# Optimization experiments

Hardware: AMD Instinct MI355X
Metric: run time of the kernel (lower is better)

The kernel has to match this reference:

```python
import jax, jax.numpy as jnp
import numpy as np

EPS = 1e-12  # matches tf l2_normalize epsilon behavior closely enough for testing

def setup_inputs() -> dict:
    key = jax.random.key(0)
    k1, k2 = jax.random.split(key)
    B, M, D = 512, 65536, 512
    context = jax.random.normal(k1, (B, D), dtype=jnp.float32)
    memory = jax.random.normal(k2, (M, D), dtype=jnp.float32)
    return {"context": context, "memory": memory}

def reference(context, memory):
    # tf.keras.losses.cosine_similarity returns NEGATIVE cosine similarity:
    # sim[b,m] = -sum(l2norm(context[b]) * l2norm(memory[m]))
    ctx_n = context / jnp.sqrt(jnp.maximum(jnp.sum(context * context, axis=-1, keepdims=True), EPS))
    mem_n = memory / jnp.sqrt(jnp.maximum(jnp.sum(memory * memory, axis=-1, keepdims=True), EPS))
    sim = -jnp.einsum('bd,md->bm', ctx_n, mem_n)  # [B, M]
    best = jnp.argmin(sim, axis=-1)               # [B], = argmax cosine
    # recall: gather then expand_dims(axis=0) -> [1, B, D]
    return memory[best][None, :, :]
```

## Files before the change

### kernel.cpp

```cpp
#include <hip/hip_runtime.h>
#include <hip/hip_bf16.h>
#include <stdint.h>

#define D_DIM 512
#define B_CTX 512
#define M_MEM 65536
#define BM 128
#define BB 128
#define BBW 256
#define BK 32
#define GBK 32
#define NIT (D_DIM / GBK)
#define LDSPAD 40
#define DELTA_COS 2.5e-3f
#define LISTCAP 2048
#define CVT_MEM_BLOCKS (M_MEM / 32)
#define CVT_BLOCKS (CVT_MEM_BLOCKS + B_CTX / 32)

typedef __attribute__((ext_vector_type(8))) short short8;
typedef __attribute__((ext_vector_type(4))) float floatx4;

__device__ __forceinline__ uint32_t f32_order(float s) {
    uint32_t u = __float_as_uint(s);
    return (u & 0x80000000u) ? ~u : (u | 0x80000000u);
}
__device__ __forceinline__ float f32_unorder(uint32_t v) {
    uint32_t u = (v & 0x80000000u) ? (v & 0x7FFFFFFFu) : ~v;
    return __uint_as_float(u);
}
__device__ __forceinline__ uint32_t pack_bf16_rtn(float a, float b) {
    uint32_t ua = __float_as_uint(a) + 0x8000u;
    uint32_t ub = __float_as_uint(b) + 0x8000u;
    return (ua >> 16) | (ub & 0xFFFF0000u);
}

typedef const __attribute__((address_space(1))) void gv_t;
typedef __attribute__((address_space(3))) void lv_t;
__device__ __forceinline__ void gload_lds16(const uint16_t* g, uint16_t* l) {
    __builtin_amdgcn_global_load_lds((gv_t*)g, (lv_t*)l, 16, 0, 0);
}

__device__ __forceinline__ bool probe_isbf(const void* memv, int* s_bf, int t) {
    if (t == 0) *s_bf = 0;
    __syncthreads();
    if (t < 64) {
        int s = 0;
        #pragma unroll
        for (int i = 0; i < 8; ++i) {
            uint32_t u = ((const uint32_t*)memv)[t * 8 + i];
            uint32_t e = (u >> 7) & 0xFFu;
            s += (e >= 96u && e <= 144u) ? 1 : 0;
        }
        atomicAdd(s_bf, s);
    }
    __syncthreads();
    return (*s_bf > 256);
}

__global__ void detect_init(const uint32_t* __restrict__ mem_raw,
                            uint32_t* __restrict__ flag) {
    __shared__ int cnt;
    if (threadIdx.x == 0) cnt = 0;
    __syncthreads();
    int s = 0;
    #pragma unroll
    for (int i = 0; i < 8; ++i) {
        uint32_t u = mem_raw[threadIdx.x * 8 + i];
        uint32_t e = (u >> 7) & 0xFFu;
        s += (e >= 96u && e <= 144u) ? 1 : 0;
    }
    atomicAdd(&cnt, s);
    __syncthreads();
    if (threadIdx.x == 0) *flag = (cnt > 256) ? 1u : 0u;
}

__global__ __launch_bounds__(256) void convert_scale(const void* __restrict__ ctxv,
                                                     const void* __restrict__ memv,
                                                     uint16_t* __restrict__ mem_s,
                                                     uint16_t* __restrict__ ctx_b) {
    __shared__ int s_bf;
    const int t = threadIdx.x;
    const bool isbf = probe_isbf(memv, &s_bf, t);
    const int lane = t & 63;
    const int w = t >> 6;
    if (blockIdx.x < CVT_MEM_BLOCKS) {
        const int r0 = (blockIdx.x * 4 + w) * 8;
        float x[8][8];
        if (isbf) {
            #pragma unroll
            for (int i = 0; i < 8; ++i) {
                uint4 v = *((const uint4*)((const uint16_t*)memv + (size_t)(r0 + i) * D_DIM) + lane);
                uint32_t ww[4] = {v.x, v.y, v.z, v.w};
                #pragma unroll
                for (int j = 0; j < 4; ++j) {
                    x[i][2 * j]     = __uint_as_float(ww[j] << 16);
                    x[i][2 * j + 1] = __uint_as_float(ww[j] & 0xFFFF0000u);
                }
            }
        } else {
            #pragma unroll
            for (int i = 0; i < 8; ++i) {
                const float4* p = (const float4*)((const float*)memv + (size_t)(r0 + i) * D_DIM) + lane * 2;
                float4 a = p[0], bq = p[1];
                x[i][0] = a.x; x[i][1] = a.y; x[i][2] = a.z; x[i][3] = a.w;
                x[i][4] = bq.x; x[i][5] = bq.y; x[i][6] = bq.z; x[i][7] = bq.w;
            }
        }
        float nsq[8];
        #pragma unroll
        for (int i = 0; i < 8; ++i) {
            float s = 0.f;
            #pragma unroll
            for (int j = 0; j < 8; ++j) s = fmaf(x[i][j], x[i][j], s);
            nsq[i] = s;
        }
        #pragma unroll
        for (int o = 32; o; o >>= 1)
            #pragma unroll
            for (int i = 0; i < 8; ++i)
                nsq[i] += __shfl_xor(nsq[i], o, 64);
        #pragma unroll
        for (int i = 0; i < 8; ++i) {
            const float invn = rsqrtf(fmaxf(nsq[i], 1e-12f));
            uint4 ov;
            ov.x = pack_bf16_rtn(x[i][0] * invn, x[i][1] * invn);
            ov.y = pack_bf16_rtn(x[i][2] * invn, x[i][3] * invn);
            ov.z = pack_bf16_rtn(x[i][4] * invn, x[i][5] * invn);
            ov.w = pack_bf16_rtn(x[i][6] * invn, x[i][7] * invn);
            *((uint4*)(mem_s + (size_t)(r0 + i) * D_DIM) + lane) = ov;
        }
    } else {
        const int r0 = ((blockIdx.x - CVT_MEM_BLOCKS) * 4 + w) * 8;
        #pragma unroll
        for (int i = 0; i < 8; ++i) {
            uint4 ov;
            if (isbf) {
                ov = *((const uint4*)((const uint16_t*)ctxv + (size_t)(r0 + i) * D_DIM) + lane);
            } else {
                const float4* p = (const float4*)((const float*)ctxv + (size_t)(r0 + i) * D_DIM) + lane * 2;
                float4 a = p[0], bq = p[1];
                ov.x = pack_bf16_rtn(a.x, a.y);
                ov.y = pack_bf16_rtn(a.z, a.w);
                ov.z = pack_bf16_rtn(bq.x, bq.y);
                ov.w = pack_bf16_rtn(bq.z, bq.w);
            }
            *((uint4*)(ctx_b + (size_t)(r0 + i) * D_DIM) + lane) = ov;
        }
    }
}

#define STAGE3(buf, kofs)                                                          \
    do {                                                                           \
        gload_lds16(ga  + (kofs), &at[buf][0][0] + (size_t)((w << 6)) * 8);        \
        gload_lds16(gb0 + (kofs), &bt[buf][0][0] + (size_t)((w << 6)) * 8);        \
        gload_lds16(gb1 + (kofs), &bt[buf][0][0] + (size_t)(512 + (w << 6)) * 8);  \
    } while (0)

__global__ __launch_bounds__(512, 4) void score_mfma(const uint16_t* __restrict__ A,
                                                     const uint16_t* __restrict__ Bc,
                                                     uint32_t* __restrict__ tmax,
                                                     int coarse) {
    __shared__ __align__(16) uint16_t at[3][BM][GBK];
    __shared__ __align__(16) uint16_t bt[3][BBW][GBK];
    __shared__ uint32_t s_gbest[8][BBW];

    const int h  = blockIdx.y * gridDim.x + blockIdx.x;
    const int v  = (h & 7) * 128 + (h >> 3);
    const int bxp = v & 1;
    const int byp = v >> 1;

    const int t    = threadIdx.x;
    const int b0   = bxp * BBW;
    const int m0   = byp * BM;
    const int lane = t & 63;
    const int w    = t >> 6;
    const int wm   = w >> 2;
    const int wb   = w & 3;
    const int quad = lane >> 4;
    const int l15  = lane & 15;
    const int scol_sw = (((t & 3) ^ ((t >> 3) & 3)) << 3);
    const int rc = ((quad ^ ((l15 >> 1) & 3)) << 3);

    const uint16_t* ga  = A  + (size_t)(m0 + (t >> 2)) * D_DIM + scol_sw;
    const uint16_t* gb0 = Bc + (size_t)(b0 + (t >> 2)) * D_DIM + scol_sw;
    const uint16_t* gb1 = gb0 + (size_t)128 * D_DIM;

    floatx4 acc[4][4];
    #pragma unroll
    for (int i = 0; i < 4; ++i)
        #pragma unroll
        for (int j = 0; j < 4; ++j)
            acc[i][j] = (floatx4){0.f, 0.f, 0.f, 0.f};

    STAGE3(0, 0);

    #pragma unroll
    for (int it = 0; it < NIT; ++it) {
        const int cur = it % 3;
        if (it < NIT - 1) STAGE3((it + 1) % 3, (it + 1) * GBK);
        if (it < NIT - 1) asm volatile("s_waitcnt vmcnt(3)" ::: "memory");
        else              asm volatile("s_waitcnt vmcnt(0)" ::: "memory");
        __builtin_amdgcn_sched_barrier(0);
        __builtin_amdgcn_s_barrier();
        __builtin_amdgcn_sched_barrier(0);

        short8 af[4], bg[4];
        #pragma unroll
        for (int i = 0; i < 4; ++i)
            af[i] = *(const short8*)&at[cur][wm * 64 + i * 16 + l15][rc];
        #pragma unroll
        for (int j = 0; j < 4; ++j)
            bg[j] = *(const short8*)&bt[cur][wb * 64 + j * 16 + l15][rc];
        __builtin_amdgcn_s_setprio(1);
        #pragma unroll
        for (int i = 0; i < 4; ++i)
            #pragma unroll
            for (int j = 0; j < 4; ++j)
                acc[i][j] = __builtin_amdgcn_mfma_f32_16x16x32_bf16(af[i], bg[j], acc[i][j], 0, 0, 0);
        __builtin_amdgcn_s_setprio(0);
    }

    #pragma unroll
    for (int i = 0; i < 4; ++i)
        #pragma unroll
        for (int j = 0; j < 4; ++j) {
            uint32_t k = 0;
            #pragma unroll
            for (int r = 0; r < 4; ++r) {
                uint32_t kk = f32_order(acc[i][j][r]);
                k = kk > k ? kk : k;
            }
            uint32_t o1 = __shfl_xor(k, 16, 64); k = o1 > k ? o1 : k;
            uint32_t o2 = __shfl_xor(k, 32, 64); k = o2 > k ? o2 : k;
            if (quad == 0) s_gbest[wm * 4 + i][wb * 64 + j * 16 + l15] = k;
        }
    __syncthreads();

    if (!coarse) {
        const int G0 = byp * 8;
        for (int e = t; e < 8 * BBW; e += 512) {
            const int col = e >> 3, g = e & 7;
            tmax[(size_t)(b0 + col) * 4096 + G0 + g] = s_gbest[g][col];
        }
    } else {
        if (t < BBW) {
            uint32_t k = s_gbest[0][t];
            #pragma unroll
            for (int g = 1; g < 8; ++g) k = s_gbest[g][t] > k ? s_gbest[g][t] : k;
            tmax[(size_t)(b0 + t) * 512 + byp] = k;
        }
    }
}

__global__ __launch_bounds__(256) void score_phase1(const void* __restrict__ ctxv,
                                                    const void* __restrict__ memv,
                                                    const uint32_t* __restrict__ flag,
                                                    uint32_t* __restrict__ tmax,
                                                    int coarse) {
    __shared__ __align__(16) uint16_t at[BM][LDSPAD];
    __shared__ __align__(16) uint16_t bt[BB][LDSPAD];
    __shared__ float s_nsq[BM];
    __shared__ uint32_t s_gbest[8][BB];

    const int t    = threadIdx.x;
    const int b0   = blockIdx.x * BB;
    const int m0   = blockIdx.y * BM;
    const int lane = t & 63;
    const int w    = t >> 6;
    const int wm   = w >> 1;
    const int wb   = w & 1;
    const int quad = lane >> 4;
    const int l15  = lane & 15;
    const int srow = t >> 2;
    const int scol = (t & 3) * 8;

    floatx4 acc[4][4];
    #pragma unroll
    for (int i = 0; i < 4; ++i)
        #pragma unroll
        for (int j = 0; j < 4; ++j)
            acc[i][j] = (floatx4){0.f, 0.f, 0.f, 0.f};

    float nsq0 = 0.f, nsq1 = 0.f;
    const bool isbf = (*flag != 0u);

    for (int k0 = 0; k0 < D_DIM; k0 += BK) {
        __syncthreads();
        if (isbf) {
            const uint16_t* mp = (const uint16_t*)memv;
            const uint16_t* cp = (const uint16_t*)ctxv;
            uint4 va0 = *(const uint4*)(mp + (size_t)(m0 + srow) * D_DIM + k0 + scol);
            uint4 va1 = *(const uint4*)(mp + (size_t)(m0 + srow + 64) * D_DIM + k0 + scol);
            uint4 vb0 = *(const uint4*)(cp + (size_t)(b0 + srow) * D_DIM + k0 + scol);
            uint4 vb1 = *(const uint4*)(cp + (size_t)(b0 + srow + 64) * D_DIM + k0 + scol);
            *(uint4*)&at[srow][scol] = va0;
            *(uint4*)&at[srow + 64][scol] = va1;
            *(uint4*)&bt[srow][scol] = vb0;
            *(uint4*)&bt[srow + 64][scol] = vb1;
            uint32_t wa0[4] = {va0.x, va0.y, va0.z, va0.w};
            uint32_t wa1[4] = {va1.x, va1.y, va1.z, va1.w};
            #pragma unroll
            for (int i = 0; i < 4; ++i) {
                float a = __uint_as_float(wa0[i] << 16);
                float b = __uint_as_float(wa0[i] & 0xFFFF0000u);
                nsq0 = fmaf(a, a, nsq0); nsq0 = fmaf(b, b, nsq0);
                float c = __uint_as_float(wa1[i] << 16);
                float d = __uint_as_float(wa1[i] & 0xFFFF0000u);
                nsq1 = fmaf(c, c, nsq1); nsq1 = fmaf(d, d, nsq1);
            }
        } else {
            const float* mp = (const float*)memv;
            const float* cp = (const float*)ctxv;
            const float4* pa0 = (const float4*)(mp + (size_t)(m0 + srow) * D_DIM + k0 + scol);
            const float4* pa1 = (const float4*)(mp + (size_t)(m0 + srow + 64) * D_DIM + k0 + scol);
            const float4* pb0 = (const float4*)(cp + (size_t)(b0 + srow) * D_DIM + k0 + scol);
            const float4* pb1 = (const float4*)(cp + (size_t)(b0 + srow + 64) * D_DIM + k0 + scol);
            float4 a0 = pa0[0], a1 = pa0[1], a2 = pa1[0], a3 = pa1[1];
            float4 c0 = pb0[0], c1 = pb0[1], c2 = pb1[0], c3 = pb1[1];
            uint4 va0 = {pack_bf16_rtn(a0.x, a0.y), pack_bf16_rtn(a0.z, a0.w),
                         pack_bf16_rtn(a1.x, a1.y), pack_bf16_rtn(a1.z, a1.w)};
            uint4 va1 = {pack_bf16_rtn(a2.x, a2.y), pack_bf16_rtn(a2.z, a2.w),
                         pack_bf16_rtn(a3.x, a3.y), pack_bf16_rtn(a3.z, a3.w)};
            uint4 vb0 = {pack_bf16_rtn(c0.x, c0.y), pack_bf16_rtn(c0.z, c0.w),
                         pack_bf16_rtn(c1.x, c1.y), pack_bf16_rtn(c1.z, c1.w)};
            uint4 vb1 = {pack_bf16_rtn(c2.x, c2.y), pack_bf16_rtn(c2.z, c2.w),
                         pack_bf16_rtn(c3.x, c3.y), pack_bf16_rtn(c3.z, c3.w)};
            *(uint4*)&at[srow][scol] = va0;
            *(uint4*)&at[srow + 64][scol] = va1;
            *(uint4*)&bt[srow][scol] = vb0;
            *(uint4*)&bt[srow + 64][scol] = vb1;
            nsq0 = fmaf(a0.x, a0.x, nsq0); nsq0 = fmaf(a0.y, a0.y, nsq0);
            nsq0 = fmaf(a0.z, a0.z, nsq0); nsq0 = fmaf(a0.w, a0.w, nsq0);
            nsq0 = fmaf(a1.x, a1.x, nsq0); nsq0 = fmaf(a1.y, a1.y, nsq0);
            nsq0 = fmaf(a1.z, a1.z, nsq0); nsq0 = fmaf(a1.w, a1.w, nsq0);
            nsq1 = fmaf(a2.x, a2.x, nsq1); nsq1 = fmaf(a2.y, a2.y, nsq1);
            nsq1 = fmaf(a2.z, a2.z, nsq1); nsq1 = fmaf(a2.w, a2.w, nsq1);
            nsq1 = fmaf(a3.x, a3.x, nsq1); nsq1 = fmaf(a3.y, a3.y, nsq1);
            nsq1 = fmaf(a3.z, a3.z, nsq1); nsq1 = fmaf(a3.w, a3.w, nsq1);
        }
        __syncthreads();

        short8 af[4], bg[4];
        #pragma unroll
        for (int i = 0; i < 4; ++i)
            af[i] = *(const short8*)&at[wm * 64 + i * 16 + l15][quad * 8];
        #pragma unroll
        for (int j = 0; j < 4; ++j)
            bg[j] = *(const short8*)&bt[wb * 64 + j * 16 + l15][quad * 8];

        #pragma unroll
        for (int i = 0; i < 4; ++i)
            #pragma unroll
            for (int j = 0; j < 4; ++j)
                acc[i][j] = __builtin_amdgcn_mfma_f32_16x16x32_bf16(af[i], bg[j], acc[i][j], 0, 0, 0);
    }

    nsq0 += __shfl_xor(nsq0, 1, 64); nsq0 += __shfl_xor(nsq0, 2, 64);
    nsq1 += __shfl_xor(nsq1, 1, 64); nsq1 += __shfl_xor(nsq1, 2, 64);
    __syncthreads();
    if ((t & 3) == 0) { s_nsq[srow] = nsq0; s_nsq[srow + 64] = nsq1; }
    __syncthreads();

    float invn[4][4];
    #pragma unroll
    for (int i = 0; i < 4; ++i)
        #pragma unroll
        for (int r = 0; r < 4; ++r)
            invn[i][r] = rsqrtf(fmaxf(s_nsq[wm * 64 + i * 16 + quad * 4 + r], 1e-12f));

    #pragma unroll
    for (int i = 0; i < 4; ++i)
        #pragma unroll
        for (int j = 0; j < 4; ++j) {
            uint32_t k = 0;
            #pragma unroll
            for (int r = 0; r < 4; ++r) {
                uint32_t kk = f32_order(acc[i][j][r] * invn[i][r]);
                k = kk > k ? kk : k;
            }
            uint32_t o1 = __shfl_xor(k, 16, 64); k = o1 > k ? o1 : k;
            uint32_t o2 = __shfl_xor(k, 32, 64); k = o2 > k ? o2 : k;
            if (quad == 0) s_gbest[wm * 4 + i][wb * 64 + j * 16 + l15] = k;
        }
    __syncthreads();

    if (!coarse) {
        const int G0 = blockIdx.y * 8;
        for (int e = t; e < 8 * BB; e += 256) {
            const int col = e >> 3, g = e & 7;
            tmax[(size_t)(b0 + col) * 4096 + G0 + g] = s_gbest[g][col];
        }
    } else {
        if (t < BB) {
            uint32_t k = s_gbest[0][t];
            #pragma unroll
            for (int g = 1; g < 8; ++g) k = s_gbest[g][t] > k ? s_gbest[g][t] : k;
            tmax[(size_t)(b0 + t) * 512 + blockIdx.y] = k;
        }
    }
}

__global__ __launch_bounds__(256) void phase2(const void* __restrict__ ctxv,
                                              const void* __restrict__ memv,
                                              const uint32_t* __restrict__ tmax,
                                              void* __restrict__ outv,
                                              int ngrp, int gshift) {
    __shared__ float s_ctx[D_DIM];
    __shared__ int s_list[LISTCAP];
    __shared__ int s_cnt;
    __shared__ int s_bf;
    __shared__ uint32_t s_red[4];
    __shared__ float s_cn[4];
    __shared__ double s_d[4], s_n[4];
    __shared__ int s_m[4];
    __shared__ int s_bestm;

    const int b = blockIdx.x;
    const int t = threadIdx.x;
    const int lane = t & 63;
    const int w = t >> 6;
    const int gmask = (1 << gshift) - 1;

    if (t == 0) s_cnt = 0;
    const bool isbf = probe_isbf(memv, &s_bf, t);

    if (isbf) {
        if (t < 64) {
            uint4 v = *((const uint4*)((const uint16_t*)ctxv + (size_t)b * D_DIM) + t);
            uint32_t ww[4] = {v.x, v.y, v.z, v.w};
            #pragma unroll
            for (int i = 0; i < 4; ++i) {
                s_ctx[t * 8 + 2 * i]     = __uint_as_float(ww[i] << 16);
                s_ctx[t * 8 + 2 * i + 1] = __uint_as_float(ww[i] & 0xFFFF0000u);
            }
        }
    } else {
        if (t < 128)
            ((float4*)s_ctx)[t] = ((const float4*)((const float*)ctxv + (size_t)b * D_DIM))[t];
    }
    __syncthreads();

    float cs = s_ctx[t] * s_ctx[t] + s_ctx[t + 256] * s_ctx[t + 256];
    #pragma unroll
    for (int o = 32; o; o >>= 1) cs += __shfl_xor(cs, o, 64);
    if (lane == 0) s_cn[w] = cs;

    const uint32_t* tk = tmax + (size_t)b * ngrp;
    uint32_t kv[16];
    uint32_t km = 0;
    const bool fine = (ngrp == 4096);
    if (fine) {
        #pragma unroll
        for (int i = 0; i < 16; ++i) kv[i] = tk[t + (i << 8)];
        #pragma unroll
        for (int i = 0; i < 16; ++i) km = kv[i] > km ? kv[i] : km;
    } else {
        #pragma unroll
        for (int i = 0; i < 2; ++i) kv[i] = tk[t + (i << 8)];
        km = kv[0] > kv[1] ? kv[0] : kv[1];
    }
    #pragma unroll
    for (int o = 32; o; o >>= 1) { uint32_t ot = __shfl_xor(km, o, 64); km = ot > km ? ot : km; }
    if (lane == 0) s_red[w] = km;
    __syncthreads();
    uint32_t kbest = s_red[0];
    #pragma unroll
    for (int i = 1; i < 4; ++i) kbest = s_red[i] > kbest ? s_red[i] : kbest;
    const float cnorm = sqrtf(s_cn[0] + s_cn[1] + s_cn[2] + s_cn[3]);
    const uint32_t keyT = f32_order(f32_unorder(kbest) - DELTA_COS * cnorm);

    if (fine) {
        #pragma unroll
        for (int i = 0; i < 16; ++i)
            if (kv[i] >= keyT) {
                int idx = atomicAdd(&s_cnt, 1);
                if (idx < LISTCAP) s_list[idx] = t + (i << 8);
            }
    } else {
        #pragma unroll
        for (int i = 0; i < 2; ++i)
            if (kv[i] >= keyT) {
                int idx = atomicAdd(&s_cnt, 1);
                if (idx < LISTCAP) s_list[idx] = t + (i << 8);
            }
    }
    __syncthreads();
    int cnt = s_cnt; if (cnt > LISTCAP) cnt = LISTCAP;
    const int total = cnt << gshift;

    double bd = -1.0e300, bn = 1.0;
    double bp = bd * 1.0e300;
    int bm = 0x7FFFFFFF;
    const float* cb = s_ctx + lane * 8;

    for (int base = w * 2; base < total; base += 8) {
        const bool has1 = (base + 1 < total);
        const int ia = base, ib = has1 ? base + 1 : base;
        const int ma = (s_list[ia >> gshift] << gshift) + (ia & gmask);
        const int mb = (s_list[ib >> gshift] << gshift) + (ib & gmask);
        double d0 = 0.0, n0 = 0.0, d1 = 0.0, n1 = 0.0;
        if (isbf) {
            uint4 va = *((const uint4*)((const uint16_t*)memv + (size_t)ma * D_DIM) + lane);
            uint4 vb = *((const uint4*)((const uint16_t*)memv + (size_t)mb * D_DIM) + lane);
            uint32_t wa[4] = {va.x, va.y, va.z, va.w};
            uint32_t wbv[4] = {vb.x, vb.y, vb.z, vb.w};
            #pragma unroll
            for (int i = 0; i < 4; ++i) {
                float a0 = __uint_as_float(wa[i] << 16);
                float a1 = __uint_as_float(wa[i] & 0xFFFF0000u);
                d0 += (double)a0 * (double)cb[2 * i];
                d0 += (double)a1 * (double)cb[2 * i + 1];
                n0 += (double)a0 * (double)a0 + (double)a1 * (double)a1;
                float b0v = __uint_as_float(wbv[i] << 16);
                float b1v = __uint_as_float(wbv[i] & 0xFFFF0000u);
                d1 += (double)b0v * (double)cb[2 * i];
                d1 += (double)b1v * (double)cb[2 * i + 1];
                n1 += (double)b0v * (double)b0v + (double)b1v * (double)b1v;
            }
        } else {
            const float4* pa = (const float4*)((const float*)memv + (size_t)ma * D_DIM) + lane * 2;
            const float4* pb = (const float4*)((const float*)memv + (size_t)mb * D_DIM) + lane * 2;
            float4 a0 = pa[0], a1 = pa[1], b0v = pb[0], b1v = pb[1];
            float xa[8] = {a0.x, a0.y, a0.z, a0.w, a1.x, a1.y, a1.z, a1.w};
            float xb[8] = {b0v.x, b0v.y, b0v.z, b0v.w, b1v.x, b1v.y, b1v.z, b1v.w};
            #pragma unroll
            for (int i = 0; i < 8; ++i) {
                d0 += (double)xa[i] * (double)cb[i];
                n0 += (double)xa[i] * (double)xa[i];
                d1 += (double)xb[i] * (double)cb[i];
                n1 += (double)xb[i] * (double)xb[i];
            }
        }
        #pragma unroll
        for (int o = 32; o; o >>= 1) {
            d0 += __shfl_xor(d0, o, 64);
            n0 += __shfl_xor(n0, o, 64);
            d1 += __shfl_xor(d1, o, 64);
            n1 += __shfl_xor(n1, o, 64);
        }
        double p0 = d0 * fabs(d0);
        double lhs = p0 * bn, rhs = bp * n0;
        if (lhs > rhs || (lhs == rhs && ma < bm)) { bd = d0; bn = n0; bp = p0; bm = ma; }
        if (has1) {
            double p1 = d1 * fabs(d1);
            double lhs1 = p1 * bn, rhs1 = bp * n1;
            if (lhs1 > rhs1 || (lhs1 == rhs1 && mb < bm)) { bd = d1; bn = n1; bp = p1; bm = mb; }
        }
    }
    if (lane == 0) { s_d[w] = bd; s_n[w] = bn; s_m[w] = bm; }
    __syncthreads();
    if (t == 0) {
        double cd = s_d[0], cn2 = s_n[0], cp = cd * fabs(cd);
        int cm = s_m[0];
        #pragma unroll
        for (int i = 1; i < 4; ++i) {
            double pd = s_d[i], pn = s_n[i], pp = pd * fabs(pd);
            double lhs = pp * cn2, rhs = cp * pn;
            if (lhs > rhs || (lhs == rhs && s_m[i] < cm)) { cd = pd; cn2 = pn; cp = pp; cm = s_m[i]; }
        }
        s_bestm = cm;
    }
    __syncthreads();
    const int mbest = s_bestm;
    if (isbf) {
        if (t < 64)
            ((uint4*)((uint16_t*)outv + (size_t)b * D_DIM))[t] =
                ((const uint4*)((const uint16_t*)memv + (size_t)mbest * D_DIM))[t];
    } else {
        if (t < 128)
            ((float4*)((float*)outv + (size_t)b * D_DIM))[t] =
                ((const float4*)((const float*)memv + (size_t)mbest * D_DIM))[t];
    }
}

extern "C" void kernel_launch(void* const* d_in, const int* in_sizes, int n_in,
                              void* d_out, int out_size, void* d_ws, size_t ws_size,
                              hipStream_t stream) {
    const void* ctx = d_in[0];
    const void* mem = d_in[1];
    if (in_sizes[0] > in_sizes[1]) { ctx = d_in[1]; mem = d_in[0]; }

    const size_t fineBytes   = (size_t)B_CTX * 4096 * 4;
    const size_t coarseBytes = (size_t)B_CTX * 512 * 4;
    const size_t ctxBytes    = (size_t)B_CTX * D_DIM * 2;
    const size_t memBytes    = (size_t)M_MEM * D_DIM * 2;
    const size_t fastBytes   = fineBytes + 256 + ctxBytes + memBytes;

    if (ws_size >= fastBytes) {
        uint32_t* tmax  = (uint32_t*)d_ws;
        uint16_t* ctx_b = (uint16_t*)((char*)d_ws + fineBytes + 256);
        uint16_t* mem_s = (uint16_t*)((char*)d_ws + fineBytes + 256 + ctxBytes);
        dim3 grid(B_CTX / BBW, M_MEM / BM);
        convert_scale<<<CVT_BLOCKS, 256, 0, stream>>>(ctx, mem, mem_s, ctx_b);
        score_mfma<<<grid, 512, 0, stream>>>(mem_s, ctx_b, tmax, 0);
        phase2<<<B_CTX, 256, 0, stream>>>(ctx, mem, tmax, d_out, 4096, 4);
    } else if (ws_size >= fineBytes + 256) {
        uint32_t* tmax = (uint32_t*)d_ws;
        uint32_t* flag = (uint32_t*)((char*)d_ws + fineBytes);
        dim3 grid(B_CTX / BB, M_MEM / BM);
        detect_init<<<1, 64, 0, stream>>>((const uint32_t*)mem, flag);
        score_phase1<<<grid, 256, 0, stream>>>(ctx, mem, flag, tmax, 0);
        phase2<<<B_CTX, 256, 0, stream>>>(ctx, mem, tmax, d_out, 4096, 4);
    } else {
        uint32_t* tmax = (uint32_t*)d_ws;
        uint32_t* flag = (uint32_t*)((char*)d_ws + coarseBytes);
        dim3 grid(B_CTX / BB, M_MEM / BM);
        detect_init<<<1, 64, 0, stream>>>((const uint32_t*)mem, flag);
        score_phase1<<<grid, 256, 0, stream>>>(ctx, mem, flag, tmax, 1);
        phase2<<<B_CTX, 256, 0, stream>>>(ctx, mem, tmax, d_out, 512, 7);
    }
}
```

Measured before the change: 263.5 us.

## Fuse memory normalization and bf16 conversion into the MFMA scoring kernel

Removes the separate pass that normalized the memory rows and wrote a bf16 copy to workspace. The scoring kernel now reads raw memory (fp32 or bf16), converts each tile to bf16 in registers and stores it to LDS, and accumulates the squared row norms along the way. It then scales the accumulated dot products by the inverse norm before the max reduction. This drops the 64MB intermediate write and read-back, but the raw memory is now read once per context-column block. The kernel also replaces the triple-buffered async LDS pipeline with a double buffer synchronised every iteration.

```diff
diff --git a/kernel.cpp b/kernel.cpp
--- a/kernel.cpp
+++ b/kernel.cpp
@@ -14,8 +14,6 @@
 #define LDSPAD 40
 #define DELTA_COS 2.5e-3f
 #define LISTCAP 2048
-#define CVT_MEM_BLOCKS (M_MEM / 32)
-#define CVT_BLOCKS (CVT_MEM_BLOCKS + B_CTX / 32)
 
 typedef __attribute__((ext_vector_type(8))) short short8;
 typedef __attribute__((ext_vector_type(4))) float floatx4;
@@ -74,117 +72,70 @@
     if (threadIdx.x == 0) *flag = (cnt > 256) ? 1u : 0u;
 }
 
-__global__ __launch_bounds__(256) void convert_scale(const void* __restrict__ ctxv,
-                                                     const void* __restrict__ memv,
-                                                     uint16_t* __restrict__ mem_s,
-                                                     uint16_t* __restrict__ ctx_b) {
+__global__ __launch_bounds__(256) void convert_ctx(const void* __restrict__ ctxv,
+                                                   const void* __restrict__ memv,
+                                                   uint16_t* __restrict__ ctx_b) {
     __shared__ int s_bf;
     const int t = threadIdx.x;
     const bool isbf = probe_isbf(memv, &s_bf, t);
     const int lane = t & 63;
     const int w = t >> 6;
-    if (blockIdx.x < CVT_MEM_BLOCKS) {
-        const int r0 = (blockIdx.x * 4 + w) * 8;
-        float x[8][8];
+    const int r0 = (blockIdx.x * 4 + w) * 8;
+    #pragma unroll
+    for (int i = 0; i < 8; ++i) {
+        uint4 ov;
         if (isbf) {
-            #pragma unroll
-            for (int i = 0; i < 8; ++i) {
-                uint4 v = *((const uint4*)((const uint16_t*)memv + (size_t)(r0 + i) * D_DIM) + lane);
-                uint32_t ww[4] = {v.x, v.y, v.z, v.w};
-                #pragma unroll
-                for (int j = 0; j < 4; ++j) {
-                    x[i][2 * j]     = __uint_as_float(ww[j] << 16);
-                    x[i][2 * j + 1] = __uint_as_float(ww[j] & 0xFFFF0000u);
-                }
-            }
+            ov = *((const uint4*)((const uint16_t*)ctxv + (size_t)(r0 + i) * D_DIM) + lane);
         } else {
-            #pragma unroll
-            for (int i = 0; i < 8; ++i) {
-                const float4* p = (const float4*)((const float*)memv + (size_t)(r0 + i) * D_DIM) + lane * 2;
-                float4 a = p[0], bq = p[1];
-                x[i][0] = a.x; x[i][1] = a.y; x[i][2] = a.z; x[i][3] = a.w;
-                x[i][4] = bq.x; x[i][5] = bq.y; x[i][6] = bq.z; x[i][7] = bq.w;
-            }
-        }
-        float nsq[8];
-        #pragma unroll
-        for (int i = 0; i < 8; ++i) {
-            float s = 0.f;
-            #pragma unroll
-            for (int j = 0; j < 8; ++j) s = fmaf(x[i][j], x[i][j], s);
-            nsq[i] = s;
-        }
-        #pragma unroll
-        for (int o = 32; o; o >>= 1)
-            #pragma unroll
-            for (int i = 0; i < 8; ++i)
-                nsq[i] += __shfl_xor(nsq[i], o, 64);
-        #pragma unroll
-        for (int i = 0; i < 8; ++i) {
-            const float invn = rsqrtf(fmaxf(nsq[i], 1e-12f));
-            uint4 ov;
-            ov.x = pack_bf16_rtn(x[i][0] * invn, x[i][1] * invn);
-            ov.y = pack_bf16_rtn(x[i][2] * invn, x[i][3] * invn);
-            ov.z = pack_bf16_rtn(x[i][4] * invn, x[i][5] * invn);
-            ov.w = pack_bf16_rtn(x[i][6] * invn, x[i][7] * invn);
-            *((uint4*)(mem_s + (size_t)(r0 + i) * D_DIM) + lane) = ov;
-        }
-    } else {
-        const int r0 = ((blockIdx.x - CVT_MEM_BLOCKS) * 4 + w) * 8;
-        #pragma unroll
-        for (int i = 0; i < 8; ++i) {
-            uint4 ov;
-            if (isbf) {
-                ov = *((const uint4*)((const uint16_t*)ctxv + (size_t)(r0 + i) * D_DIM) + lane);
-            } else {
-                const float4* p = (const float4*)((const float*)ctxv + (size_t)(r0 + i) * D_DIM) + lane * 2;
-                float4 a = p[0], bq = p[1];
-                ov.x = pack_bf16_rtn(a.x, a.y);
-                ov.y = pack_bf16_rtn(a.z, a.w);
-                ov.z = pack_bf16_rtn(bq.x, bq.y);
-                ov.w = pack_bf16_rtn(bq.z, bq.w);
-            }
-            *((uint4*)(ctx_b + (size_t)(r0 + i) * D_DIM) + lane) = ov;
-        }
-    }
-}
-
-#define STAGE3(buf, kofs)                                                          \
-    do {                                                                           \
-        gload_lds16(ga  + (kofs), &at[buf][0][0] + (size_t)((w << 6)) * 8);        \
-        gload_lds16(gb0 + (kofs), &bt[buf][0][0] + (size_t)((w << 6)) * 8);        \
-        gload_lds16(gb1 + (kofs), &bt[buf][0][0] + (size_t)(512 + (w << 6)) * 8);  \
-    } while (0)
-
-__global__ __launch_bounds__(512, 4) void score_mfma(const uint16_t* __restrict__ A,
-                                                     const uint16_t* __restrict__ Bc,
-                                                     uint32_t* __restrict__ tmax,
-                                                     int coarse) {
-    __shared__ __align__(16) uint16_t at[3][BM][GBK];
-    __shared__ __align__(16) uint16_t bt[3][BBW][GBK];
+            const float4* p = (const float4*)((const float*)ctxv + (size_t)(r0 + i) * D_DIM) + lane * 2;
+            float4 a = p[0], bq = p[1];
+            ov.x = pack_bf16_rtn(a.x, a.y);
+            ov.y = pack_bf16_rtn(a.z, a.w);
+            ov.z = pack_bf16_rtn(bq.x, bq.y);
+            ov.w = pack_bf16_rtn(bq.z, bq.w);
+        }
+        *((uint4*)(ctx_b + (size_t)(r0 + i) * D_DIM) + lane) = ov;
+    }
+}
+
+__global__ __launch_bounds__(512, 4) void score_fused(const void* __restrict__ memv,
+                                                      const uint16_t* __restrict__ Bc,
+                                                      uint32_t* __restrict__ tmax,
+                                                      int coarse) {
+    __shared__ __align__(16) uint16_t at[2][BM][GBK];
+    __shared__ __align__(16) uint16_t bt[2][BBW][GBK];
     __shared__ uint32_t s_gbest[8][BBW];
+    __shared__ float s_nsq[BM];
+    __shared__ int s_bf;
+
+    const int t = threadIdx.x;
+    const bool isbf = probe_isbf(memv, &s_bf, t);
 
     const int h  = blockIdx.y * gridDim.x + blockIdx.x;
     const int v  = (h & 7) * 128 + (h >> 3);
     const int bxp = v & 1;
     const int byp = v >> 1;
-
-    const int t    = threadIdx.x;
-    const int b0   = bxp * BBW;
-    const int m0   = byp * BM;
+    const int b0  = bxp * BBW;
+    const int m0  = byp * BM;
     const int lane = t & 63;
     const int w    = t >> 6;
     const int wm   = w >> 2;
     const int wb   = w & 3;
     const int quad = lane >> 4;
     const int l15  = lane & 15;
+
+    const int arow = t >> 2;
+    const int achk = t & 3;
+    const int aswz = achk ^ ((arow >> 1) & 3);
     const int scol_sw = (((t & 3) ^ ((t >> 3) & 3)) << 3);
     const int rc = ((quad ^ ((l15 >> 1) & 3)) << 3);
 
-    const uint16_t* ga  = A  + (size_t)(m0 + (t >> 2)) * D_DIM + scol_sw;
     const uint16_t* gb0 = Bc + (size_t)(b0 + (t >> 2)) * D_DIM + scol_sw;
     const uint16_t* gb1 = gb0 + (size_t)128 * D_DIM;
-
+    const float*    gaf = (const float*)memv + (size_t)(m0 + arow) * D_DIM + achk * 8;
+    const uint16_t* gab = (const uint16_t*)memv + (size_t)(m0 + arow) * D_DIM + achk * 8;
+
+    float nsq = 0.f;
     floatx4 acc[4][4];
     #pragma unroll
     for (int i = 0; i < 4; ++i)
@@ -192,18 +143,38 @@
         for (int j = 0; j < 4; ++j)
             acc[i][j] = (floatx4){0.f, 0.f, 0.f, 0.f};
 
-    STAGE3(0, 0);
+    {
+        gload_lds16(gb0, &bt[0][0][0] + (size_t)(w << 6) * 8);
+        gload_lds16(gb1, &bt[0][0][0] + (size_t)(512 + (w << 6)) * 8);
+        uint4 av;
+        float xs[8];
+        if (isbf) {
+            av = *(const uint4*)gab;
+            uint32_t ww[4] = {av.x, av.y, av.z, av.w};
+            #pragma unroll
+            for (int j = 0; j < 4; ++j) {
+                xs[2 * j]     = __uint_as_float(ww[j] << 16);
+                xs[2 * j + 1] = __uint_as_float(ww[j] & 0xFFFF0000u);
+            }
+        } else {
+            float4 fa = *(const float4*)gaf;
+            float4 fb = *(const float4*)(gaf + 4);
+            xs[0] = fa.x; xs[1] = fa.y; xs[2] = fa.z; xs[3] = fa.w;
+            xs[4] = fb.x; xs[5] = fb.y; xs[6] = fb.z; xs[7] = fb.w;
+            av.x = pack_bf16_rtn(xs[0], xs[1]);
+            av.y = pack_bf16_rtn(xs[2], xs[3]);
+            av.z = pack_bf16_rtn(xs[4], xs[5]);
+            av.w = pack_bf16_rtn(xs[6], xs[7]);
+        }
+        #pragma unroll
+        for (int j = 0; j < 8; ++j) nsq = fmaf(xs[j], xs[j], nsq);
+        *(uint4*)&at[0][arow][aswz * 8] = av;
+        __syncthreads();
+    }
 
     #pragma unroll
     for (int it = 0; it < NIT; ++it) {
-        const int cur = it % 3;
-        if (it < NIT - 1) STAGE3((it + 1) % 3, (it + 1) * GBK);
-        if (it < NIT - 1) asm volatile("s_waitcnt vmcnt(3)" ::: "memory");
-        else              asm volatile("s_waitcnt vmcnt(0)" ::: "memory");
-        __builtin_amdgcn_sched_barrier(0);
-        __builtin_amdgcn_s_barrier();
-        __builtin_amdgcn_sched_barrier(0);
-
+        const int cur = it & 1;
         short8 af[4], bg[4];
         #pragma unroll
         for (int i = 0; i < 4; ++i)
@@ -211,6 +182,23 @@
         #pragma unroll
         for (int j = 0; j < 4; ++j)
             bg[j] = *(const short8*)&bt[cur][wb * 64 + j * 16 + l15][rc];
+
+        uint4 av;
+        float xs[8];
+        if (it < NIT - 1) {
+            const int ko = (it + 1) * GBK;
+            gload_lds16(gb0 + ko, &bt[cur ^ 1][0][0] + (size_t)(w << 6) * 8);
+            gload_lds16(gb1 + ko, &bt[cur ^ 1][0][0] + (size_t)(512 + (w << 6)) * 8);
+            if (isbf) {
+                av = *(const uint4*)(gab + ko);
+            } else {
+                float4 fa = *(const float4*)(gaf + ko);
+                float4 fb = *(const float4*)(gaf + ko + 4);
+                xs[0] = fa.x; xs[1] = fa.y; xs[2] = fa.z; xs[3] = fa.w;
+                xs[4] = fb.x; xs[5] = fb.y; xs[6] = fb.z; xs[7] = fb.w;
+            }
+        }
+
         __builtin_amdgcn_s_setprio(1);
         #pragma unroll
         for (int i = 0; i < 4; ++i)
@@ -218,7 +206,39 @@
             for (int j = 0; j < 4; ++j)
                 acc[i][j] = __builtin_amdgcn_mfma_f32_16x16x32_bf16(af[i], bg[j], acc[i][j], 0, 0, 0);
         __builtin_amdgcn_s_setprio(0);
-    }
+
+        if (it < NIT - 1) {
+            if (isbf) {
+                uint32_t ww[4] = {av.x, av.y, av.z, av.w};
+                #pragma unroll
+                for (int j = 0; j < 4; ++j) {
+                    xs[2 * j]     = __uint_as_float(ww[j] << 16);
+                    xs[2 * j + 1] = __uint_as_float(ww[j] & 0xFFFF0000u);
+                }
+            } else {
+                av.x = pack_bf16_rtn(xs[0], xs[1]);
+                av.y = pack_bf16_rtn(xs[2], xs[3]);
+                av.z = pack_bf16_rtn(xs[4], xs[5]);
+                av.w = pack_bf16_rtn(xs[6], xs[7]);
+            }
+            #pragma unroll
+            for (int j = 0; j < 8; ++j) nsq = fmaf(xs[j], xs[j], nsq);
+            *(uint4*)&at[cur ^ 1][arow][aswz * 8] = av;
+        }
+        __syncthreads();
+    }
+
+    nsq += __shfl_xor(nsq, 1, 64);
+    nsq += __shfl_xor(nsq, 2, 64);
+    if ((t & 3) == 0) s_nsq[arow] = nsq;
+    __syncthreads();
+
+    float invn[4][4];
+    #pragma unroll
+    for (int i = 0; i < 4; ++i)
+        #pragma unroll
+        for (int r = 0; r < 4; ++r)
+            invn[i][r] = rsqrtf(fmaxf(s_nsq[wm * 64 + i * 16 + quad * 4 + r], 1e-12f));
 
     #pragma unroll
     for (int i = 0; i < 4; ++i)
@@ -227,7 +247,7 @@
             uint32_t k = 0;
             #pragma unroll
             for (int r = 0; r < 4; ++r) {
-                uint32_t kk = f32_order(acc[i][j][r]);
+                uint32_t kk = f32_order(acc[i][j][r] * invn[i][r]);
                 k = kk > k ? kk : k;
             }
             uint32_t o1 = __shfl_xor(k, 16, 64); k = o1 > k ? o1 : k;
@@ -583,16 +603,14 @@
     const size_t fineBytes   = (size_t)B_CTX * 4096 * 4;
     const size_t coarseBytes = (size_t)B_CTX * 512 * 4;
     const size_t ctxBytes    = (size_t)B_CTX * D_DIM * 2;
-    const size_t memBytes    = (size_t)M_MEM * D_DIM * 2;
-    const size_t fastBytes   = fineBytes + 256 + ctxBytes + memBytes;
+    const size_t fastBytes   = fineBytes + 256 + ctxBytes;
 
     if (ws_size >= fastBytes) {
         uint32_t* tmax  = (uint32_t*)d_ws;
         uint16_t* ctx_b = (uint16_t*)((char*)d_ws + fineBytes + 256);
-        uint16_t* mem_s = (uint16_t*)((char*)d_ws + fineBytes + 256 + ctxBytes);
         dim3 grid(B_CTX / BBW, M_MEM / BM);
-        convert_scale<<<CVT_BLOCKS, 256, 0, stream>>>(ctx, mem, mem_s, ctx_b);
-        score_mfma<<<grid, 512, 0, stream>>>(mem_s, ctx_b, tmax, 0);
+        convert_ctx<<<16, 256, 0, stream>>>(ctx, mem, ctx_b);
+        score_fused<<<grid, 512, 0, stream>>>(mem, ctx_b, tmax, 0);
         phase2<<<B_CTX, 256, 0, stream>>>(ctx, mem, tmax, d_out, 4096, 4);
     } else if (ws_size >= fineBytes + 256) {
         uint32_t* tmax = (uint32_t*)d_ws;
```

Measured after the change: 282.9 us. +7.4%, slower.
